# Performance work log

Hardware: AMD Instinct MI355X
Metric: run time of the kernel (lower is better)

The kernel has to match this reference:

```python
import jax, jax.numpy as jnp
import numpy as np
from jax import lax

C, NH, HC, HID, P = 192, 8, 64, 512, 16
B, H, W = 2, 128, 128
EPS = 1e-5


def setup_inputs() -> dict:
    key = jax.random.key(0)
    ks = jax.random.split(key, 12)
    f = lambda i, shape: jax.random.normal(ks[i], shape, jnp.float32) * 0.05
    return dict(
        x=jax.random.normal(ks[0], (B, C, H, W), jnp.float32),
        ln1_g=jnp.ones((C,), jnp.float32), ln1_b=jnp.zeros((C,), jnp.float32),
        wq=f(1, (HID, C)), wk=f(2, (HID, C)), wv=f(3, (HID, C)),
        wo=f(4, (C, HID)), bo=jnp.zeros((C,), jnp.float32),
        dw_w=f(5, (C, 1, 3, 3)), dw_b=jnp.zeros((C,), jnp.float32),
        mlp_w=f(6, (C, 2 * C)), mlp_b=jnp.zeros((C,), jnp.float32),
        ln2_g=jnp.ones((C,), jnp.float32), ln2_b=jnp.zeros((C,), jnp.float32),
        c1_w=f(7, (C, C)), c1_b=jnp.zeros((C,), jnp.float32),
        res_w=f(8, (C, 1, 3, 3)), res_b=jnp.zeros((C,), jnp.float32),
        c2_w=f(9, (C, C)), c2_b=jnp.zeros((C,), jnp.float32),
    )


def ln_ch(x, g, b):
    # LayerNorm over the channel dim of an NCHW tensor (biased variance, like torch)
    m = x.mean(1, keepdims=True)
    v = ((x - m) ** 2).mean(1, keepdims=True)
    return (x - m) / jnp.sqrt(v + EPS) * g[None, :, None, None] + b[None, :, None, None]


def inorm(x):
    # InstanceNorm2d, affine=False
    m = x.mean((2, 3), keepdims=True)
    v = ((x - m) ** 2).mean((2, 3), keepdims=True)
    return (x - m) / jnp.sqrt(v + EPS)


def conv1x1(x, w, b=None):
    y = jnp.einsum('oc,bchw->bohw', w, x)
    return y if b is None else y + b[None, :, None, None]


def dwconv(x, w, b):
    y = lax.conv_general_dilated(x, w, (1, 1), 'SAME',
                                 feature_group_count=x.shape[1],
                                 dimension_numbers=('NCHW', 'OIHW', 'NCHW'))
    return y + b[None, :, None, None]


def res_block(x, w, b):
    return jax.nn.gelu(inorm(dwconv(x, w, b)), approximate=False) + x


def dpsa(x, ln_g, ln_b, wq, wk, wv, wo, bo):
    Bs, _, Hs, Ws = x.shape
    xn = ln_ch(x, ln_g, ln_b)

    def proj(w):  # -> (B*NH, H, W, HC)
        t = jnp.einsum('oc,bchw->bohw', w, xn)
        return t.reshape(Bs * NH, HC, Hs, Ws).transpose(0, 2, 3, 1)

    l2n = lambda t: t / jnp.maximum(jnp.linalg.norm(t, axis=-1, keepdims=True), 1e-12)
    q = l2n(proj(wq))
    k = l2n(proj(wk))
    v = proj(wv)

    qs = q.sum((1, 2))                                   # (BH, HC)
    h_scores = jnp.einsum('bc,bhc->bh', qs, k.sum(2))    # (BH, H)
    w_scores = jnp.einsum('bc,bwc->bw', qs, k.sum(1))    # (BH, W)
    _, h_idx = lax.top_k(h_scores, P)
    _, w_idx = lax.top_k(w_scores, P)

    k = jnp.take_along_axis(k, h_idx[:, :, None, None], axis=1)   # (BH, P, W, HC)
    v = jnp.take_along_axis(v, h_idx[:, :, None, None], axis=1)
    k = jnp.take_along_axis(k, w_idx[:, None, :, None], axis=2)   # (BH, P, P, HC)
    v = jnp.take_along_axis(v, w_idx[:, None, :, None], axis=2)

    qf = q.reshape(Bs * NH, Hs * Ws, HC)
    kf = k.reshape(Bs * NH, P * P, HC)
    vf = v.reshape(Bs * NH, P * P, HC)
    attn = jax.nn.softmax(jnp.einsum('bqc,bkc->bqk', qf, kf), axis=-1)
    out = jnp.einsum('bqk,bkc->bqc', attn, vf)
    out = out.reshape(Bs, NH, Hs, Ws, HC).transpose(0, 1, 4, 2, 3).reshape(Bs, NH * HC, Hs, Ws)
    return conv1x1(out, wo, bo)


def reference(x, ln1_g, ln1_b, wq, wk, wv, wo, bo, dw_w, dw_b, mlp_w, mlp_b,
              ln2_g, ln2_b, c1_w, c1_b, res_w, res_b, c2_w, c2_b):
    global_branch = dpsa(x, ln1_g, ln1_b, wq, wk, wv, wo, bo)
    local_branch = dwconv(x, dw_w, dw_b)
    f = jnp.concatenate((local_branch, global_branch), axis=1)
    f = conv1x1(f, mlp_w, mlp_b) + x
    y = ln_ch(f, ln2_g, ln2_b)
    y = jax.nn.gelu(inorm(conv1x1(y, c1_w, c1_b)), approximate=False)
    y = res_block(y, res_w, res_b)
    y = inorm(conv1x1(y, c2_w, c2_b))
    return y
```

## Files before the change

kernel.cpp:

```cpp
#include <hip/hip_runtime.h>
#include <math.h>

constexpr int kC   = 192;
constexpr int kNH  = 8;
constexpr int kHC  = 64;
constexpr int kHID = 512;
constexpr int kP   = 16;
constexpr int kB   = 2;
constexpr int kH   = 128;
constexpr int kW   = 128;
constexpr int kHW  = kH * kW;
constexpr int kN   = kB * kHW;
constexpr float kEPS = 1e-5f;

typedef __attribute__((ext_vector_type(8))) short bf16x8;
typedef __attribute__((ext_vector_type(4))) float f32x4;

__device__ inline unsigned short f2bf(float f) {
    unsigned int u = __builtin_bit_cast(unsigned int, f);
    unsigned int r = (u + 0x7FFFu + ((u >> 16) & 1u)) >> 16;
    return (unsigned short)r;
}
__device__ inline float bf2f(unsigned short u) {
    return __builtin_bit_cast(float, (unsigned int)u << 16);
}
__device__ inline unsigned int cvtpk(float lo, float hi) {
    unsigned int r;
    asm("v_cvt_pk_bf16_f32 %0, %1, %2" : "=v"(r) : "v"(lo), "v"(hi));
    return r;
}
__device__ inline unsigned long long pk4(float a, float b, float c, float d) {
    return (unsigned long long)cvtpk(a, b) | ((unsigned long long)cvtpk(c, d) << 32);
}
__device__ inline f32x4 ubf4(unsigned long long u) {
    f32x4 r;
    r[0] = bf2f((unsigned short)u);
    r[1] = bf2f((unsigned short)(u >> 16));
    r[2] = bf2f((unsigned short)(u >> 32));
    r[3] = bf2f((unsigned short)(u >> 48));
    return r;
}

__global__ void prep_kernel(float* __restrict__ acc,
                            const float* wq, const float* wk, const float* wm,
                            const float* c1, const float* c2,
                            unsigned short* wqb, unsigned short* wkb,
                            unsigned short* mlpb1, unsigned short* c1b, unsigned short* c2b)
{
    int i = blockIdx.x * 256 + threadIdx.x;
    if (i < 2304) { acc[i] = 0.f; return; }
    i -= 2304;
    if (i < 98304) { wqb[i] = f2bf(wq[i]); return; }
    i -= 98304;
    if (i < 98304) { wkb[i] = f2bf(wk[i]); return; }
    i -= 98304;
    if (i < 36864) { int o = i / 192, k = i - o * 192; mlpb1[i] = f2bf(wm[o * 384 + k]); return; }
    i -= 36864;
    if (i < 36864) { c1b[i] = f2bf(c1[i]); return; }
    i -= 36864;
    if (i < 36864) { c2b[i] = f2bf(c2[i]); return; }
}

__global__ void wfuse_kernel(const float* __restrict__ mlp_w, const float* __restrict__ wo,
                             const float* __restrict__ mlp_b, const float* __restrict__ bo,
                             unsigned short* __restrict__ w2pb, float* __restrict__ bp2)
{
    int i = blockIdx.x * 256 + threadIdx.x;
    int o = i >> 9, j = i & 511;
    const float* a = mlp_w + o * 384 + 192;
    float s = 0.f;
    for (int c = 0; c < 192; ++c) s += a[c] * wo[c * 512 + j];
    w2pb[o * 512 + j] = f2bf(s);
    if (j == 0) {
        float t = mlp_b[o];
        for (int c = 0; c < 192; ++c) t += a[c] * bo[c];
        bp2[o] = t;
    }
}

__global__ __launch_bounds__(256) void txln_kernel(const float* __restrict__ x,
                                                   unsigned short* __restrict__ xpb,
                                                   unsigned short* __restrict__ xnb,
                                                   const float* __restrict__ g,
                                                   const float* __restrict__ bb)
{
    __shared__ float tile[192][65];
    __shared__ float red[2][4][64];
    __shared__ float pms[64], prs[64];
    int hw0 = blockIdx.x * 64;
    int b   = blockIdx.y;
    int tid = threadIdx.x;
    for (int i = tid; i < 192 * 64; i += 256) {
        int c = i >> 6, p = i & 63;
        tile[c][p] = x[(size_t)(b * kC + c) * kHW + hw0 + p];
    }
    __syncthreads();
    {
        int p = tid & 63, qt = tid >> 6;
        float s = 0.f, ss = 0.f;
// ... 54 lines not shown
#define MGEMM_CORE(KVAL, APTR, BPTR)                                              \
    {                                                                             \
        const unsigned short* Ap = APTR;                                          \
        const unsigned short* Bp = BPTR;                                          \
        _Pragma("unroll 2")                                                       \
        for (int k = 0; k < KVAL; k += 32) {                                      \
            bf16x8 a0 = *(const bf16x8*)(Ap + k);                                 \
            bf16x8 a1 = *(const bf16x8*)(Ap + (size_t)16 * KVAL + k);             \
            bf16x8 b0 = *(const bf16x8*)(Bp + k);                                 \
            bf16x8 b1 = *(const bf16x8*)(Bp + (size_t)16 * KVAL + k);             \
            bf16x8 b2 = *(const bf16x8*)(Bp + (size_t)32 * KVAL + k);             \
            bf16x8 b3 = *(const bf16x8*)(Bp + (size_t)48 * KVAL + k);             \
            acc[0][0] = __builtin_amdgcn_mfma_f32_16x16x32_bf16(a0, b0, acc[0][0], 0, 0, 0); \
            acc[0][1] = __builtin_amdgcn_mfma_f32_16x16x32_bf16(a0, b1, acc[0][1], 0, 0, 0); \
            acc[0][2] = __builtin_amdgcn_mfma_f32_16x16x32_bf16(a0, b2, acc[0][2], 0, 0, 0); \
            acc[0][3] = __builtin_amdgcn_mfma_f32_16x16x32_bf16(a0, b3, acc[0][3], 0, 0, 0); \
            acc[1][0] = __builtin_amdgcn_mfma_f32_16x16x32_bf16(a1, b0, acc[1][0], 0, 0, 0); \
            acc[1][1] = __builtin_amdgcn_mfma_f32_16x16x32_bf16(a1, b1, acc[1][1], 0, 0, 0); \
            acc[1][2] = __builtin_amdgcn_mfma_f32_16x16x32_bf16(a1, b2, acc[1][2], 0, 0, 0); \
            acc[1][3] = __builtin_amdgcn_mfma_f32_16x16x32_bf16(a1, b3, acc[1][3], 0, 0, 0); \
        }                                                                         \
    }

__global__ __launch_bounds__(256) void mgemm_is_kernel(
    const unsigned short* __restrict__ A, const unsigned short* __restrict__ B,
    unsigned short* __restrict__ out, const float* __restrict__ bias,
    float* __restrict__ accp)
{
    __shared__ float sa[2][64], qa[2][64];
    int nB = blockIdx.x * 128, oB = blockIdx.y * 64;
    int w = threadIdx.x >> 6, lane = threadIdx.x & 63;
    int l15 = lane & 15, g = lane >> 4;
    int wm = w & 1, wn = w >> 1;

    f32x4 acc[2][4];
#pragma unroll
    for (int mt = 0; mt < 2; ++mt)
#pragma unroll
        for (int nt = 0; nt < 4; ++nt) acc[mt][nt] = (f32x4){0.f,0.f,0.f,0.f};

    MGEMM_CORE(192, A + (size_t)(oB + wm * 32 + l15) * 192 + 8 * g,
                    B + (size_t)(nB + wn * 64 + l15) * 192 + 8 * g);

    f32x4 vv[2][4];
#pragma unroll
    for (int mt = 0; mt < 2; ++mt)
// ... 55 lines not shown

    f32x4 acc[2][4];
#pragma unroll
    for (int mt = 0; mt < 2; ++mt)
#pragma unroll
        for (int nt = 0; nt < 4; ++nt) acc[mt][nt] = (f32x4){0.f,0.f,0.f,0.f};

    MGEMM_CORE(192, A1 + (size_t)(oB + wm * 32 + l15) * 192 + 8 * g,
                    B1 + (size_t)(nB + wn * 64 + l15) * 192 + 8 * g);
    MGEMM_CORE(512, A2 + (size_t)(oB + wm * 32 + l15) * 512 + 8 * g,
                    B2 + (size_t)(nB + wn * 64 + l15) * 512 + 8 * g);

#pragma unroll
    for (int mt = 0; mt < 2; ++mt)
#pragma unroll
        for (int nt = 0; nt < 4; ++nt) {
            int o = oB + wm * 32 + mt * 16 + 4 * g;
            int n = nB + wn * 64 + nt * 16 + l15;
            f32x4 v = acc[mt][nt];
            v[0] += bp2[o]; v[1] += bp2[o+1]; v[2] += bp2[o+2]; v[3] += bp2[o+3];
            v += ubf4(*(const unsigned long long*)(res + (size_t)n * kC + o));
            *(unsigned long long*)(out + (size_t)n * kC + o) = pk4(v[0], v[1], v[2], v[3]);
        }
}

__global__ __launch_bounds__(256) void mgemm_l2_kernel(
    const unsigned short* __restrict__ A, const unsigned short* __restrict__ B,
    unsigned short* __restrict__ out, float* __restrict__ red_out)
{
    __shared__ float ssq[2][2][4][16];
    __shared__ float rbuf[2][2][4][2][4];
    int nB = blockIdx.x * 128, oB = blockIdx.y * 64;
    int w = threadIdx.x >> 6, lane = threadIdx.x & 63;
    int l15 = lane & 15, g = lane >> 4;
    int wm = w & 1, wn = w >> 1;

    f32x4 acc[2][4];
#pragma unroll
    for (int mt = 0; mt < 2; ++mt)
#pragma unroll
        for (int nt = 0; nt < 4; ++nt) acc[mt][nt] = (f32x4){0.f,0.f,0.f,0.f};

    MGEMM_CORE(192, A + (size_t)(oB + wm * 32 + l15) * 192 + 8 * g,
                    B + (size_t)(nB + wn * 64 + l15) * 192 + 8 * g);

#pragma unroll
    for (int nt = 0; nt < 4; ++nt) {
        float s = 0.f;
#pragma unroll
        for (int mt = 0; mt < 2; ++mt) {
            f32x4 a = acc[mt][nt];
            s += (a[0]*a[0] + a[1]*a[1]) + (a[2]*a[2] + a[3]*a[3]);
        }
        s += __shfl_xor(s, 16);
        s += __shfl_xor(s, 32);
        if (g == 0) ssq[wm][wn][nt][l15] = s;
    }
    __syncthreads();

    float sc[4];
#pragma unroll
    for (int nt = 0; nt < 4; ++nt) {
        float ss2 = ssq[0][wn][nt][l15] + ssq[1][wn][nt][l15];
        sc[nt] = 1.0f / fmaxf(sqrtf(ss2), 1e-12f);
    }

#pragma unroll
    for (int nt = 0; nt < 4; ++nt) {
        int n = nB + wn * 64 + nt * 16 + l15;
#pragma unroll
        for (int mt = 0; mt < 2; ++mt) {
            int o = oB + wm * 32 + mt * 16 + 4 * g;
            f32x4 v = acc[mt][nt];
            *(unsigned long long*)(out + (size_t)n * kHID + o) =
                pk4(v[0]*sc[nt], v[1]*sc[nt], v[2]*sc[nt], v[3]*sc[nt]);
        }
    }

    float sred[2][4] = {};
#pragma unroll
    for (int nt = 0; nt < 4; ++nt)
#pragma unroll
        for (int mt = 0; mt < 2; ++mt) {
            f32x4 a = acc[mt][nt];
            sred[mt][0] += a[0] * sc[nt];
            sred[mt][1] += a[1] * sc[nt];
            sred[mt][2] += a[2] * sc[nt];
            sred[mt][3] += a[3] * sc[nt];
        }
#pragma unroll
    for (int off = 1; off < 16; off <<= 1)
#pragma unroll
        for (int mt = 0; mt < 2; ++mt)
#pragma unroll
            for (int r = 0; r < 4; ++r)
                sred[mt][r] += __shfl_xor(sred[mt][r], off);
    if (l15 == 0)
#pragma unroll
        for (int mt = 0; mt < 2; ++mt)
#pragma unroll
            for (int r = 0; r < 4; ++r)
                rbuf[wm][wn][g][mt][r] = sred[mt][r];
    __syncthreads();
    if (threadIdx.x < 64) {
        int o = threadIdx.x;
        int wm2 = o >> 5, mt2 = (o >> 4) & 1, g2 = (o >> 2) & 3, r2 = o & 3;
        float v = rbuf[wm2][0][g2][mt2][r2] + rbuf[wm2][1][g2][mt2][r2];
        int row = (nB & (kHW - 1)) >> 7;
        int b = nB >> 14;
        int bh = b * 8 + blockIdx.y;
        red_out[((size_t)(bh * 128 + row)) * 64 + o] = v;
    }
}

__global__ void sum_h_kernel(const unsigned short* __restrict__ buf, float* __restrict__ out)
{
    __shared__ float red[4][64];
    int w = blockIdx.x, bh = blockIdx.y;
    int hc = threadIdx.x & 63, seg = threadIdx.x >> 6;
    int b = bh >> 3, nh = bh & 7;
    const unsigned short* p = buf + (size_t)(b * kHW + seg * 32 * kW + w) * kHID + nh * kHC + hc;
    float s = 0.f;
    for (int h = 0; h < 32; ++h) s += bf2f(p[(size_t)h * kW * kHID]);
    red[seg][hc] = s;
    __syncthreads();
    if (threadIdx.x < 64)
        out[((size_t)bh * kW + w) * kHC + threadIdx.x] =
            red[0][threadIdx.x] + red[1][threadIdx.x] + red[2][threadIdx.x] + red[3][threadIdx.x];
}

__global__ void score_topk_kernel(const float* __restrict__ qpart,
                                  const float* __restrict__ ksum_h,
                                  const float* __restrict__ ksum_w,
                                  int* __restrict__ hidx, int* __restrict__ widx)
{
    __shared__ float qsl[2][64];
    __shared__ float hs[128], ws[128];
    int bh = blockIdx.x;
    int tid = threadIdx.x;
    int hc = tid & 63, grp = tid >> 6;
    {
        const float* qp = qpart + ((size_t)bh * 128 + grp * 64) * 64 + hc;
        float s = 0.f;
        for (int i = 0; i < 64; ++i) s += qp[(size_t)i * 64];
        qsl[grp][hc] = s;
    }
    __syncthreads();
    if (tid < 64) qsl[0][tid] += qsl[1][tid];
    __syncthreads();
    {
        const float* kh = ksum_h + ((size_t)bh * 128 + tid) * 64;
// ... 8 lines not shown
    }
    __syncthreads();
    int sel = tid >> 6;
    const float* sc = sel ? ws : hs;
    int* out = (sel ? widx : hidx) + bh * kP;
    int lane = tid & 63;
    float v0 = sc[lane], v1 = sc[lane + 64];
    int i0 = lane, i1 = lane + 64;
    for (int p = 0; p < kP; ++p) {
        float bv; int bi;
        if (v1 > v0) { bv = v1; bi = i1; } else { bv = v0; bi = i0; }
#pragma unroll
        for (int off = 1; off < 64; off <<= 1) {
            float ov = __shfl_xor(bv, off);
            int   oi = __shfl_xor(bi, off);
            if (ov > bv || (ov == bv && oi < bi)) { bv = ov; bi = oi; }
        }
        if (lane == 0) out[p] = bi;
        if (i0 == bi) v0 = -INFINITY;
        if (i1 == bi) v1 = -INFINITY;
    }
}

__global__ void gather_kv_kernel(const unsigned short* __restrict__ kpb,
                                 const unsigned short* __restrict__ xnb,
                                 const float* __restrict__ wv,
                                 const int* __restrict__ hidx, const int* __restrict__ widx,
                                 unsigned short* __restrict__ kf, unsigned short* __restrict__ vfT)
{
    int bh = blockIdx.y, p1 = blockIdx.x;
    int b = bh >> 3, nh = bh & 7;
    int hc = threadIdx.x & 63, pg = threadIdx.x >> 6;
    int hrow = hidx[bh * kP + p1];
    int o = nh * kHC + hc;
    const float* wvp = wv + (size_t)o * kC;
    for (int p2 = pg; p2 < kP; p2 += 4) {
        int wcol = widx[bh * kP + p2];
        int n = b * kHW + hrow * kW + wcol;
        int kidx = p1 * kP + p2;
        kf[((size_t)bh * 256 + kidx) * 64 + hc] = kpb[(size_t)n * kHID + nh * kHC + hc];
        const unsigned int* xr = (const unsigned int*)(xnb + (size_t)n * kC);
        float s = 0.f;
        for (int c2 = 0; c2 < kC / 2; ++c2) {
            unsigned int u = xr[c2];
            s += wvp[c2 * 2]     * bf2f((unsigned short)(u & 0xffff));
            s += wvp[c2 * 2 + 1] * bf2f((unsigned short)(u >> 16));
        }
        vfT[((size_t)bh * 64 + hc) * 256 + kidx] = f2bf(s);
    }
}

__global__ __launch_bounds__(256) void attn_kernel(
    const unsigned short* __restrict__ qpb, unsigned short* __restrict__ ob,
    const unsigned short* __restrict__ kf, const unsigned short* __restrict__ vfT)
{
    __shared__ unsigned short pls[64 * 256];
    __shared__ float lred[4][4][16];

    int bh = blockIdx.y; int b = bh >> 3, nh = bh & 7;
    int n0 = b * kHW + blockIdx.x * 64;
    int tid = threadIdx.x;
    int w = tid >> 6, lane = tid & 63, l15 = lane & 15, g = lane >> 4;

    bf16x8 bq[4][2];
#pragma unroll
    for (int nt = 0; nt < 4; ++nt)
#pragma unroll
        for (int kt = 0; kt < 2; ++kt)
            bq[nt][kt] = *(const bf16x8*)(qpb + (size_t)(n0 + nt * 16 + l15) * kHID
                                          + nh * kHC + kt * 32 + 8 * g);

    const unsigned short* kfb = kf + (size_t)bh * 256 * 64;
    bf16x8 ak[4][2];
#pragma unroll
    for (int mt = 0; mt < 4; ++mt)
#pragma unroll
        for (int kt = 0; kt < 2; ++kt)
            ak[mt][kt] = *(const bf16x8*)&kfb[(size_t)(w * 64 + mt * 16 + l15) * 64 + kt * 32 + 8 * g];

    f32x4 acc[4][4];
#pragma unroll
    for (int mt = 0; mt < 4; ++mt)
#pragma unroll
        for (int nt = 0; nt < 4; ++nt) acc[mt][nt] = (f32x4){0.f,0.f,0.f,0.f};

#pragma unroll
    for (int kt = 0; kt < 2; ++kt)
#pragma unroll
        for (int mt = 0; mt < 4; ++mt)
#pragma unroll
            for (int nt = 0; nt < 4; ++nt)
                acc[mt][nt] = __builtin_amdgcn_mfma_f32_16x16x32_bf16(
                    ak[mt][kt], bq[nt][kt], acc[mt][nt], 0, 0, 0);

    float lpart[4] = {0.f, 0.f, 0.f, 0.f};
#pragma unroll
    for (int mt = 0; mt < 4; ++mt)
#pragma unroll
        for (int nt = 0; nt < 4; ++nt) {
            float e0 = __expf(acc[mt][nt][0]);
            float e1 = __expf(acc[mt][nt][1]);
            float e2 = __expf(acc[mt][nt][2]);
            float e3 = __expf(acc[mt][nt][3]);
            lpart[nt] += (e0 + e1) + (e2 + e3);
            int qq = nt * 16 + l15;
            int k0 = w * 64 + mt * 16 + 4 * g;
            int kx = k0 ^ ((qq & 7) << 3);
            *(unsigned long long*)&pls[qq * 256 + kx] = pk4(e0, e1, e2, e3);
        }
#pragma unroll
    for (int nt = 0; nt < 4; ++nt) {
        lpart[nt] += __shfl_xor(lpart[nt], 16);
        lpart[nt] += __shfl_xor(lpart[nt], 32);
    }
    if (g == 0)
#pragma unroll
        for (int nt = 0; nt < 4; ++nt) lred[w][nt][l15] = lpart[nt];
    __syncthreads();

    const unsigned short* vfb = vfT + (size_t)bh * 64 * 256;
    f32x4 oacc[4];
#pragma unroll
    for (int nt = 0; nt < 4; ++nt) oacc[nt] = (f32x4){0.f,0.f,0.f,0.f};

#pragma unroll
    for (int ks = 0; ks < 8; ++ks) {
        bf16x8 av = *(const bf16x8*)&vfb[(size_t)(w * 16 + l15) * 256 + ks * 32 + 8 * g];
#pragma unroll
        for (int nt = 0; nt < 4; ++nt) {
            int qq = nt * 16 + l15;
            int kx = (ks * 32 + 8 * g) ^ ((qq & 7) << 3);
            bf16x8 bp = *(const bf16x8*)&pls[qq * 256 + kx];
            oacc[nt] = __builtin_amdgcn_mfma_f32_16x16x32_bf16(av, bp, oacc[nt], 0, 0, 0);
        }
    }

#pragma unroll
    for (int nt = 0; nt < 4; ++nt) {
        float l = lred[0][nt][l15] + lred[1][nt][l15] + lred[2][nt][l15] + lred[3][nt][l15];
        float inv = 1.0f / l;
        int qq = nt * 16 + l15;
        int hc0 = w * 16 + 4 * g;
        *(unsigned long long*)(ob + (size_t)(n0 + qq) * kHID + nh * kHC + hc0) =
            pk4(oacc[nt][0] * inv, oacc[nt][1] * inv, oacc[nt][2] * inv, oacc[nt][3] * inv);
    }
}

__global__ void dwconv_pm_kernel(const unsigned short* __restrict__ in,
                                 unsigned short* __restrict__ out,
                                 const float* __restrict__ wt, const float* __restrict__ bias)
{
    int idx = blockIdx.x * 256 + threadIdx.x;
    int n = idx / 48;
    int c0 = (idx - n * 48) * 4;
    int hw = n & (kHW - 1);
    int h = hw >> 7, ww = hw & 127;
    f32x4 s = *(const f32x4*)(bias + c0);
#pragma unroll
    for (int dy = -1; dy <= 1; ++dy) {
        int hh = h + dy;
        if (hh < 0 || hh >= kH) continue;
#pragma unroll
        for (int dx = -1; dx <= 1; ++dx) {
            int wx = ww + dx;
            if (wx < 0 || wx >= kW) continue;
            f32x4 v = ubf4(*(const unsigned long long*)(in + (size_t)(n + dy * kW + dx) * kC + c0));
            int t = (dy + 1) * 3 + (dx + 1);
            s[0] += v[0] * wt[(c0 + 0) * 9 + t];
            s[1] += v[1] * wt[(c0 + 1) * 9 + t];
            s[2] += v[2] * wt[(c0 + 2) * 9 + t];
            s[3] += v[3] * wt[(c0 + 3) * 9 + t];
        }
    }
    *(unsigned long long*)(out + (size_t)n * kC + c0) = pk4(s[0], s[1], s[2], s[3]);
}

__global__ void istats_bf16_kernel(const unsigned short* __restrict__ in, float* __restrict__ acc)
{
    int n0 = blockIdx.x * 64;
    int b = n0 >> 14;
    int c = threadIdx.x;
    float s = 0.f, ss = 0.f;
    for (int p = 0; p < 64; ++p) {
        float v = bf2f(in[(size_t)(n0 + p) * kC + c]);
        s += v; ss += v * v;
    }
    atomicAdd(&acc[(size_t)(b * kC + c) * 2],     s);
    atomicAdd(&acc[(size_t)(b * kC + c) * 2 + 1], ss);
}

__device__ inline void inorm_ms(const float* acc, int b, int c, float& m, float& rs)
{
    float s  = acc[(size_t)(b * kC + c) * 2];
    float ss = acc[(size_t)(b * kC + c) * 2 + 1];
    m = s * (1.0f / kHW);
    float var = ss * (1.0f / kHW) - m * m;
    rs = rsqrtf(var + kEPS);
}

template<int MODE>
__global__ void apply_pm_kernel(const unsigned short* __restrict__ in, const float* __restrict__ acc,
                                unsigned short* __restrict__ out, const unsigned short* __restrict__ addsrc)
{
    int idx = blockIdx.x * 256 + threadIdx.x;
    int n = idx / 48;
    int c0 = (idx - n * 48) * 4;
    int b = n >> 14;
    f32x4 v = ubf4(*(const unsigned long long*)(in + (size_t)n * kC + c0));
    f32x4 r;
#pragma unroll
    for (int j = 0; j < 4; ++j) {
        float m, rs;
        inorm_ms(acc, b, c0 + j, m, rs);
        float x = (v[j] - m) * rs;
        r[j] = 0.5f * x * (1.0f + erff(x * 0.70710678118654752f));
    }
    if (MODE == 1)
        r += ubf4(*(const unsigned long long*)(addsrc + (size_t)n * kC + c0));
    *(unsigned long long*)(out + (size_t)n * kC + c0) = pk4(r[0], r[1], r[2], r[3]);
}

__global__ __launch_bounds__(256) void final_kernel(const unsigned short* __restrict__ in,
                                                    const float* __restrict__ acc,
                                                    float* __restrict__ out)
{
    __shared__ unsigned short tile[192][68];
    int n0 = blockIdx.x * 64;
    int b = n0 >> 14;
    int hw0 = n0 & (kHW - 1);
    int tid = threadIdx.x;
    for (int i = tid; i < 64 * 48; i += 256) {
        int p = i / 48, cq = i - p * 48;
        unsigned long long u = *(const unsigned long long*)(in + (size_t)(n0 + p) * kC + cq * 4);
        tile[cq * 4 + 0][p] = (unsigned short)u;
        tile[cq * 4 + 1][p] = (unsigned short)(u >> 16);
        tile[cq * 4 + 2][p] = (unsigned short)(u >> 32);
        tile[cq * 4 + 3][p] = (unsigned short)(u >> 48);
    }
    __syncthreads();
    for (int i = tid; i < 192 * 16; i += 256) {
        int c = i >> 4, grp = i & 15;
        float m, rs;
// ... 17 lines not shown
    const float* wk    = (const float*)d_in[4];
    const float* wv    = (const float*)d_in[5];
    const float* wo    = (const float*)d_in[6];
    const float* bo    = (const float*)d_in[7];
    const float* dw_w  = (const float*)d_in[8];
    const float* dw_b  = (const float*)d_in[9];
    const float* mlp_w = (const float*)d_in[10];
    const float* mlp_b = (const float*)d_in[11];
    const float* ln2_g = (const float*)d_in[12];
    const float* ln2_b = (const float*)d_in[13];
    const float* c1_w  = (const float*)d_in[14];
    const float* c1_b  = (const float*)d_in[15];
    const float* res_w = (const float*)d_in[16];
    const float* res_b = (const float*)d_in[17];
    const float* c2_w  = (const float*)d_in[18];
    const float* c2_b  = (const float*)d_in[19];

    char* base = (char*)d_ws;
    unsigned short* XPb = (unsigned short*)(base);
    unsigned short* XNb = (unsigned short*)(base + 25165824);
    unsigned short* QPb = (unsigned short*)(base + 37748736);
    unsigned short* F   = QPb;
    unsigned short* T2  = QPb;
    unsigned short* KPb = (unsigned short*)(base + 71303168);
    unsigned short* OB  = KPb;
    unsigned short* Y2  = KPb;
    unsigned short* LB  = (unsigned short*)(base + 104857600);
    unsigned short* Y3  = LB;
    unsigned short* T1  = (unsigned short*)(base + 117440512);
    unsigned short* R   = T1;
    char* sm = base + 130023424;
    float* qpart  = (float*)(sm);                 sm += 524288;
    float* ksum_h = (float*)(sm);                 sm += 524288;
    float* ksum_w = (float*)(sm);                 sm += 524288;
    float* acc0   = (float*)(sm);                 sm += 3072;
    float* acc1   = (float*)(sm);                 sm += 3072;
    float* acc2   = (float*)(sm);                 sm += 3072;
    unsigned short* kf   = (unsigned short*)(sm); sm += 524288;
    unsigned short* vfT  = (unsigned short*)(sm); sm += 524288;
    unsigned short* wqb  = (unsigned short*)(sm); sm += 196608;
    unsigned short* wkb  = (unsigned short*)(sm); sm += 196608;
    unsigned short* mlpb1= (unsigned short*)(sm); sm += 73728;
    unsigned short* c1b  = (unsigned short*)(sm); sm += 73728;
    unsigned short* c2b  = (unsigned short*)(sm); sm += 73728;
    unsigned short* w2pb = (unsigned short*)(sm); sm += 196608;
    float* bp2 = (float*)(sm);                    sm += 1024;
    int* hidx = (int*)(sm);                       sm += 1024;
    int* widx = (int*)(sm);

    prep_kernel<<<1209, 256, 0, stream>>>(acc0, wq, wk, mlp_w, c1_w, c2_w,
                                          wqb, wkb, mlpb1, c1b, c2b);
    wfuse_kernel<<<384, 256, 0, stream>>>(mlp_w, wo, mlp_b, bo, w2pb, bp2);
    txln_kernel<<<dim3(kHW / 64, kB), 256, 0, stream>>>(x, XPb, XNb, ln1_g, ln1_b);

    mgemm_l2_kernel<<<dim3(kN / 128, kNH), 256, 0, stream>>>(wqb, XNb, QPb, qpart);
    mgemm_l2_kernel<<<dim3(kN / 128, kNH), 256, 0, stream>>>(wkb, XNb, KPb, ksum_h);
    sum_h_kernel<<<dim3(kW, 16), 256, 0, stream>>>(KPb, ksum_w);
    score_topk_kernel<<<16, 128, 0, stream>>>(qpart, ksum_h, ksum_w, hidx, widx);
    gather_kv_kernel<<<dim3(kP, 16), 256, 0, stream>>>(KPb, XNb, wv, hidx, widx, kf, vfT);
    attn_kernel<<<dim3(kHW / 64, 16), 256, 0, stream>>>(QPb, OB, kf, vfT);

    dwconv_pm_kernel<<<(kN * 48) / 256, 256, 0, stream>>>(XPb, LB, dw_w, dw_b);
    mgemm_mlp_kernel<<<dim3(kN / 128, kC / 64), 256, 0, stream>>>(mlpb1, LB, w2pb, OB, F, bp2, XPb);

    ln_pm_bf16_kernel<<<(kN * 4) / 256, 256, 0, stream>>>(F, XNb, ln2_g, ln2_b);
    mgemm_is_kernel<<<dim3(kN / 128, kC / 64), 256, 0, stream>>>(c1b, XNb, T1, c1_b, acc0);
    apply_pm_kernel<0><<<(kN * 48) / 256, 256, 0, stream>>>(T1, acc0, Y2, nullptr);
    dwconv_pm_kernel<<<(kN * 48) / 256, 256, 0, stream>>>(Y2, R, res_w, res_b);
    istats_bf16_kernel<<<kN / 64, 192, 0, stream>>>(R, acc1);
    apply_pm_kernel<1><<<(kN * 48) / 256, 256, 0, stream>>>(R, acc1, Y3, Y2);
    mgemm_is_kernel<<<dim3(kN / 128, kC / 64), 256, 0, stream>>>(c2b, Y3, T2, c2_b, acc2);
    final_kernel<<<kN / 64, 256, 0, stream>>>(T2, acc2, (float*)d_out);
}
```

Before: 490.0 us.

## Fuse branch GEMMs and dwconv, drop K-projection buffer, fold GELU into convs

```diff
diff --git a/kernel.cpp b/kernel.cpp
--- a/kernel.cpp
+++ b/kernel.cpp
@@ -40,16 +40,21 @@
     r[3] = bf2f((unsigned short)(u >> 48));
     return r;
 }
-
-__global__ void prep_kernel(float* __restrict__ acc,
+__device__ inline float gelu_f(float x) {
+    return 0.5f * x * (1.0f + erff(x * 0.70710678118654752f));
+}
+
+__global__ void prep_kernel(float* __restrict__ zbase,
                             const float* wq, const float* wk, const float* wm,
                             const float* c1, const float* c2,
+                            const float* wo, const float* mlp_b, const float* bo,
                             unsigned short* wqb, unsigned short* wkb,
-                            unsigned short* mlpb1, unsigned short* c1b, unsigned short* c2b)
+                            unsigned short* mlpb1, unsigned short* c1b, unsigned short* c2b,
+                            unsigned short* w2pb, float* bp2)
 {
     int i = blockIdx.x * 256 + threadIdx.x;
-    if (i < 2304) { acc[i] = 0.f; return; }
-    i -= 2304;
+    if (i < 133376) { zbase[i] = 0.f; return; }
+    i -= 133376;
     if (i < 98304) { wqb[i] = f2bf(wq[i]); return; }
     i -= 98304;
     if (i < 98304) { wkb[i] = f2bf(wk[i]); return; }
@@ -59,22 +64,18 @@
     if (i < 36864) { c1b[i] = f2bf(c1[i]); return; }
     i -= 36864;
     if (i < 36864) { c2b[i] = f2bf(c2[i]); return; }
-}
-
-__global__ void wfuse_kernel(const float* __restrict__ mlp_w, const float* __restrict__ wo,
-                             const float* __restrict__ mlp_b, const float* __restrict__ bo,
-                             unsigned short* __restrict__ w2pb, float* __restrict__ bp2)
-{
-    int i = blockIdx.x * 256 + threadIdx.x;
-    int o = i >> 9, j = i & 511;
-    const float* a = mlp_w + o * 384 + 192;
-    float s = 0.f;
-    for (int c = 0; c < 192; ++c) s += a[c] * wo[c * 512 + j];
-    w2pb[o * 512 + j] = f2bf(s);
-    if (j == 0) {
-        float t = mlp_b[o];
-        for (int c = 0; c < 192; ++c) t += a[c] * bo[c];
-        bp2[o] = t;
+    i -= 36864;
+    if (i < 98304) {
+        int o = i >> 9, j = i & 511;
+        const float* a = wm + o * 384 + 192;
+        float s = 0.f;
+        for (int c = 0; c < 192; ++c) s += a[c] * wo[c * 512 + j];
+        w2pb[o * 512 + j] = f2bf(s);
+        if (j == 0) {
+            float t = mlp_b[o];
+            for (int c = 0; c < 192; ++c) t += a[c] * bo[c];
+            bp2[o] = t;
+        }
     }
 }
 
@@ -175,6 +176,155 @@
         }                                                                         \
     }
 
+template<int IS_K>
+__device__ void mgemm_l2_body(int nblk, int head,
+                              const unsigned short* __restrict__ A,
+                              const unsigned short* __restrict__ B,
+                              unsigned short* __restrict__ out,
+                              float* __restrict__ red_out,
+                              float* __restrict__ ksum_w)
+{
+    __shared__ float ssq[2][2][4][16];
+    __shared__ float rbuf[2][2][4][2][4];
+    int nB = nblk * 128, oB = head * 64;
+    int w = threadIdx.x >> 6, lane = threadIdx.x & 63;
+    int l15 = lane & 15, g = lane >> 4;
+    int wm = w & 1, wn = w >> 1;
+
+    f32x4 acc[2][4];
+#pragma unroll
+    for (int mt = 0; mt < 2; ++mt)
+#pragma unroll
+        for (int nt = 0; nt < 4; ++nt) acc[mt][nt] = (f32x4){0.f,0.f,0.f,0.f};
+
+    MGEMM_CORE(192, A + (size_t)(oB + wm * 32 + l15) * 192 + 8 * g,
+                    B + (size_t)(nB + wn * 64 + l15) * 192 + 8 * g);
+
+#pragma unroll
+    for (int nt = 0; nt < 4; ++nt) {
+        float s = 0.f;
+#pragma unroll
+        for (int mt = 0; mt < 2; ++mt) {
+            f32x4 a = acc[mt][nt];
+            s += (a[0]*a[0] + a[1]*a[1]) + (a[2]*a[2] + a[3]*a[3]);
+        }
+        s += __shfl_xor(s, 16);
+        s += __shfl_xor(s, 32);
+        if (g == 0) ssq[wm][wn][nt][l15] = s;
+    }
+    __syncthreads();
+
+    float sc[4];
+#pragma unroll
+    for (int nt = 0; nt < 4; ++nt) {
+        float ss2 = ssq[0][wn][nt][l15] + ssq[1][wn][nt][l15];
+        sc[nt] = 1.0f / fmaxf(sqrtf(ss2), 1e-12f);
+    }
+
+    int b = nB >> 14;
+    int bh = b * 8 + head;
+#pragma unroll
+    for (int nt = 0; nt < 4; ++nt) {
+        int n = nB + wn * 64 + nt * 16 + l15;
+#pragma unroll
+        for (int mt = 0; mt < 2; ++mt) {
+            int o = oB + wm * 32 + mt * 16 + 4 * g;
+            f32x4 v = acc[mt][nt];
+            if (IS_K) {
+                int ww = n & (kW - 1);
+                float* dst = ksum_w + ((size_t)(bh * kW + ww)) * 64 + (o & 63);
+                atomicAdd(dst + 0, v[0] * sc[nt]);
+                atomicAdd(dst + 1, v[1] * sc[nt]);
+                atomicAdd(dst + 2, v[2] * sc[nt]);
+                atomicAdd(dst + 3, v[3] * sc[nt]);
+            } else {
+                *(unsigned long long*)(out + (size_t)n * kHID + o) =
+                    pk4(v[0]*sc[nt], v[1]*sc[nt], v[2]*sc[nt], v[3]*sc[nt]);
+            }
+        }
+    }
+
+    float sred[2][4] = {};
+#pragma unroll
+    for (int nt = 0; nt < 4; ++nt)
+#pragma unroll
+        for (int mt = 0; mt < 2; ++mt) {
+            f32x4 a = acc[mt][nt];
+            sred[mt][0] += a[0] * sc[nt];
+            sred[mt][1] += a[1] * sc[nt];
+            sred[mt][2] += a[2] * sc[nt];
+            sred[mt][3] += a[3] * sc[nt];
+        }
+#pragma unroll
+    for (int off = 1; off < 16; off <<= 1)
+#pragma unroll
+        for (int mt = 0; mt < 2; ++mt)
+#pragma unroll
+            for (int r = 0; r < 4; ++r)
+                sred[mt][r] += __shfl_xor(sred[mt][r], off);
+    if (l15 == 0)
+#pragma unroll
+        for (int mt = 0; mt < 2; ++mt)
+#pragma unroll
+            for (int r = 0; r < 4; ++r)
+                rbuf[wm][wn][g][mt][r] = sred[mt][r];
+    __syncthreads();
+    if (threadIdx.x < 64) {
+        int o = threadIdx.x;
+        int wm2 = o >> 5, mt2 = (o >> 4) & 1, g2 = (o >> 2) & 3, r2 = o & 3;
+        float v = rbuf[wm2][0][g2][mt2][r2] + rbuf[wm2][1][g2][mt2][r2];
+        int row = (nB & (kHW - 1)) >> 7;
+        red_out[((size_t)(bh * 128 + row)) * 64 + o] = v;
+    }
+}
+
+__device__ void dwconv_body(int idx, const unsigned short* __restrict__ in,
+                            unsigned short* __restrict__ out,
+                            const float* __restrict__ wt, const float* __restrict__ bias)
+{
+    int n = idx / 48;
+    int c0 = (idx - n * 48) * 4;
+    int hw = n & (kHW - 1);
+    int h = hw >> 7, ww = hw & 127;
+    f32x4 s = *(const f32x4*)(bias + c0);
+#pragma unroll
+    for (int dy = -1; dy <= 1; ++dy) {
+        int hh = h + dy;
+        if (hh < 0 || hh >= kH) continue;
+#pragma unroll
+        for (int dx = -1; dx <= 1; ++dx) {
+            int wx = ww + dx;
+            if (wx < 0 || wx >= kW) continue;
+            f32x4 v = ubf4(*(const unsigned long long*)(in + (size_t)(n + dy * kW + dx) * kC + c0));
+            int t = (dy + 1) * 3 + (dx + 1);
+            s[0] += v[0] * wt[(c0 + 0) * 9 + t];
+            s[1] += v[1] * wt[(c0 + 1) * 9 + t];
+            s[2] += v[2] * wt[(c0 + 2) * 9 + t];
+            s[3] += v[3] * wt[(c0 + 3) * 9 + t];
+        }
+    }
+    *(unsigned long long*)(out + (size_t)n * kC + c0) = pk4(s[0], s[1], s[2], s[3]);
+}
+
+__global__ __launch_bounds__(256) void branch_kernel(
+    const unsigned short* __restrict__ wqb, const unsigned short* __restrict__ wkb,
+    const unsigned short* __restrict__ xnb, const unsigned short* __restrict__ xpb,
+    unsigned short* __restrict__ qpb, float* __restrict__ qpart,
+    float* __restrict__ ksum_h, float* __restrict__ ksum_w,
+    unsigned short* __restrict__ lb,
+    const float* __restrict__ dw_w, const float* __restrict__ dw_b)
+{
+    int id = blockIdx.x;
+    if (id < 2048) {
+        mgemm_l2_body<0>(id & 255, id >> 8, wqb, xnb, qpb, qpart, nullptr);
+    } else if (id < 4096) {
+        id -= 2048;
+        mgemm_l2_body<1>(id & 255, id >> 8, wkb, xnb, nullptr, ksum_h, ksum_w);
+    } else {
+        dwconv_body((id - 4096) * 256 + threadIdx.x, xpb, lb, dw_w, dw_b);
+    }
+}
+
 __global__ __launch_bounds__(256) void mgemm_is_kernel(
     const unsigned short* __restrict__ A, const unsigned short* __restrict__ B,
     unsigned short* __restrict__ out, const float* __restrict__ bias,
@@ -276,111 +426,6 @@
             v += ubf4(*(const unsigned long long*)(res + (size_t)n * kC + o));
             *(unsigned long long*)(out + (size_t)n * kC + o) = pk4(v[0], v[1], v[2], v[3]);
         }
-}
-
-__global__ __launch_bounds__(256) void mgemm_l2_kernel(
-    const unsigned short* __restrict__ A, const unsigned short* __restrict__ B,
-    unsigned short* __restrict__ out, float* __restrict__ red_out)
-{
-    __shared__ float ssq[2][2][4][16];
-    __shared__ float rbuf[2][2][4][2][4];
-    int nB = blockIdx.x * 128, oB = blockIdx.y * 64;
-    int w = threadIdx.x >> 6, lane = threadIdx.x & 63;
-    int l15 = lane & 15, g = lane >> 4;
-    int wm = w & 1, wn = w >> 1;
-
-    f32x4 acc[2][4];
-#pragma unroll
-    for (int mt = 0; mt < 2; ++mt)
-#pragma unroll
-        for (int nt = 0; nt < 4; ++nt) acc[mt][nt] = (f32x4){0.f,0.f,0.f,0.f};
-
-    MGEMM_CORE(192, A + (size_t)(oB + wm * 32 + l15) * 192 + 8 * g,
-                    B + (size_t)(nB + wn * 64 + l15) * 192 + 8 * g);
-
-#pragma unroll
-    for (int nt = 0; nt < 4; ++nt) {
-        float s = 0.f;
-#pragma unroll
-        for (int mt = 0; mt < 2; ++mt) {
-            f32x4 a = acc[mt][nt];
-            s += (a[0]*a[0] + a[1]*a[1]) + (a[2]*a[2] + a[3]*a[3]);
-        }
-        s += __shfl_xor(s, 16);
-        s += __shfl_xor(s, 32);
-        if (g == 0) ssq[wm][wn][nt][l15] = s;
-    }
-    __syncthreads();
-
-    float sc[4];
-#pragma unroll
-    for (int nt = 0; nt < 4; ++nt) {
-        float ss2 = ssq[0][wn][nt][l15] + ssq[1][wn][nt][l15];
-        sc[nt] = 1.0f / fmaxf(sqrtf(ss2), 1e-12f);
-    }
-
-#pragma unroll
-    for (int nt = 0; nt < 4; ++nt) {
-        int n = nB + wn * 64 + nt * 16 + l15;
-#pragma unroll
-        for (int mt = 0; mt < 2; ++mt) {
-            int o = oB + wm * 32 + mt * 16 + 4 * g;
-            f32x4 v = acc[mt][nt];
-            *(unsigned long long*)(out + (size_t)n * kHID + o) =
-                pk4(v[0]*sc[nt], v[1]*sc[nt], v[2]*sc[nt], v[3]*sc[nt]);
-        }
-    }
-
-    float sred[2][4] = {};
-#pragma unroll
-    for (int nt = 0; nt < 4; ++nt)
-#pragma unroll
-        for (int mt = 0; mt < 2; ++mt) {
-            f32x4 a = acc[mt][nt];
-            sred[mt][0] += a[0] * sc[nt];
-            sred[mt][1] += a[1] * sc[nt];
-            sred[mt][2] += a[2] * sc[nt];
-            sred[mt][3] += a[3] * sc[nt];
-        }
-#pragma unroll
-    for (int off = 1; off < 16; off <<= 1)
-#pragma unroll
-        for (int mt = 0; mt < 2; ++mt)
-#pragma unroll
-            for (int r = 0; r < 4; ++r)
-                sred[mt][r] += __shfl_xor(sred[mt][r], off);
-    if (l15 == 0)
-#pragma unroll
-        for (int mt = 0; mt < 2; ++mt)
-#pragma unroll
-            for (int r = 0; r < 4; ++r)
-                rbuf[wm][wn][g][mt][r] = sred[mt][r];
-    __syncthreads();
-    if (threadIdx.x < 64) {
-        int o = threadIdx.x;
-        int wm2 = o >> 5, mt2 = (o >> 4) & 1, g2 = (o >> 2) & 3, r2 = o & 3;
-        float v = rbuf[wm2][0][g2][mt2][r2] + rbuf[wm2][1][g2][mt2][r2];
-        int row = (nB & (kHW - 1)) >> 7;
-        int b = nB >> 14;
-        int bh = b * 8 + blockIdx.y;
-        red_out[((size_t)(bh * 128 + row)) * 64 + o] = v;
-    }
-}
-
-__global__ void sum_h_kernel(const unsigned short* __restrict__ buf, float* __restrict__ out)
-{
-    __shared__ float red[4][64];
-    int w = blockIdx.x, bh = blockIdx.y;
-    int hc = threadIdx.x & 63, seg = threadIdx.x >> 6;
-    int b = bh >> 3, nh = bh & 7;
-    const unsigned short* p = buf + (size_t)(b * kHW + seg * 32 * kW + w) * kHID + nh * kHC + hc;
-    float s = 0.f;
-    for (int h = 0; h < 32; ++h) s += bf2f(p[(size_t)h * kW * kHID]);
-    red[seg][hc] = s;
-    __syncthreads();
-    if (threadIdx.x < 64)
-        out[((size_t)bh * kW + w) * kHC + threadIdx.x] =
-            red[0][threadIdx.x] + red[1][threadIdx.x] + red[2][threadIdx.x] + red[3][threadIdx.x];
 }
 
 __global__ void score_topk_kernel(const float* __restrict__ qpart,
@@ -435,7 +480,7 @@
     }
 }
 
-__global__ void gather_kv_kernel(const unsigned short* __restrict__ kpb,
+__global__ void gather_kv_kernel(const unsigned short* __restrict__ wkb,
                                  const unsigned short* __restrict__ xnb,
                                  const float* __restrict__ wv,
                                  const int* __restrict__ hidx, const int* __restrict__ widx,
@@ -447,19 +492,29 @@
     int hrow = hidx[bh * kP + p1];
     int o = nh * kHC + hc;
     const float* wvp = wv + (size_t)o * kC;
+    const unsigned short* wkp = wkb + (size_t)o * kC;
     for (int p2 = pg; p2 < kP; p2 += 4) {
         int wcol = widx[bh * kP + p2];
         int n = b * kHW + hrow * kW + wcol;
         int kidx = p1 * kP + p2;
-        kf[((size_t)bh * 256 + kidx) * 64 + hc] = kpb[(size_t)n * kHID + nh * kHC + hc];
         const unsigned int* xr = (const unsigned int*)(xnb + (size_t)n * kC);
-        float s = 0.f;
+        const unsigned int* kr = (const unsigned int*)wkp;
+        float sv = 0.f, sk = 0.f;
         for (int c2 = 0; c2 < kC / 2; ++c2) {
             unsigned int u = xr[c2];
-            s += wvp[c2 * 2]     * bf2f((unsigned short)(u & 0xffff));
-            s += wvp[c2 * 2 + 1] * bf2f((unsigned short)(u >> 16));
-        }
-        vfT[((size_t)bh * 64 + hc) * 256 + kidx] = f2bf(s);
+            float x0 = bf2f((unsigned short)(u & 0xffff));
+            float x1 = bf2f((unsigned short)(u >> 16));
+            sv += wvp[c2 * 2] * x0 + wvp[c2 * 2 + 1] * x1;
+            unsigned int kw2 = kr[c2];
+            sk += bf2f((unsigned short)(kw2 & 0xffff)) * x0
+                + bf2f((unsigned short)(kw2 >> 16)) * x1;
+        }
+        float ss = sk * sk;
+#pragma unroll
+        for (int off = 1; off < 64; off <<= 1) ss += __shfl_xor(ss, off);
+        float sc = 1.0f / fmaxf(sqrtf(ss), 1e-12f);
+        kf[((size_t)bh * 256 + kidx) * 64 + hc] = f2bf(sk * sc);
+        vfT[((size_t)bh * 64 + hc) * 256 + kidx] = f2bf(sv);
     }
 }
 
@@ -471,18 +526,10 @@
     __shared__ float lred[4][4][16];
 
     int bh = blockIdx.y; int b = bh >> 3, nh = bh & 7;
-    int n0 = b * kHW + blockIdx.x * 64;
+    int nbase = b * kHW + blockIdx.x * 128;
     int tid = threadIdx.x;
     int w = tid >> 6, lane = tid & 63, l15 = lane & 15, g = lane >> 4;
 
-    bf16x8 bq[4][2];
-#pragma unroll
-    for (int nt = 0; nt < 4; ++nt)
-#pragma unroll
-        for (int kt = 0; kt < 2; ++kt)
-            bq[nt][kt] = *(const bf16x8*)(qpb + (size_t)(n0 + nt * 16 + l15) * kHID
-                                          + nh * kHC + kt * 32 + 8 * g);
-
     const unsigned short* kfb = kf + (size_t)bh * 256 * 64;
     bf16x8 ak[4][2];
 #pragma unroll
@@ -491,101 +538,87 @@
         for (int kt = 0; kt < 2; ++kt)
             ak[mt][kt] = *(const bf16x8*)&kfb[(size_t)(w * 64 + mt * 16 + l15) * 64 + kt * 32 + 8 * g];
 
-    f32x4 acc[4][4];
-#pragma unroll
-    for (int mt = 0; mt < 4; ++mt)
-#pragma unroll
-        for (int nt = 0; nt < 4; ++nt) acc[mt][nt] = (f32x4){0.f,0.f,0.f,0.f};
-
-#pragma unroll
-    for (int kt = 0; kt < 2; ++kt)
+    const unsigned short* vfb = vfT + (size_t)bh * 64 * 256;
+
+#pragma unroll
+    for (int sub = 0; sub < 2; ++sub) {
+        int n0 = nbase + sub * 64;
+        bf16x8 bq[4][2];
+#pragma unroll
+        for (int nt = 0; nt < 4; ++nt)
+#pragma unroll
+            for (int kt = 0; kt < 2; ++kt)
+                bq[nt][kt] = *(const bf16x8*)(qpb + (size_t)(n0 + nt * 16 + l15) * kHID
+                                              + nh * kHC + kt * 32 + 8 * g);
+
+        f32x4 acc[4][4];
 #pragma unroll
         for (int mt = 0; mt < 4; ++mt)
 #pragma unroll
-            for (int nt = 0; nt < 4; ++nt)
-                acc[mt][nt] = __builtin_amdgcn_mfma_f32_16x16x32_bf16(
-                    ak[mt][kt], bq[nt][kt], acc[mt][nt], 0, 0, 0);
-
-    float lpart[4] = {0.f, 0.f, 0.f, 0.f};
-#pragma unroll
-    for (int mt = 0; mt < 4; ++mt)
+            for (int nt = 0; nt < 4; ++nt) acc[mt][nt] = (f32x4){0.f,0.f,0.f,0.f};
+
+#pragma unroll
+        for (int kt = 0; kt < 2; ++kt)
+#pragma unroll
+            for (int mt = 0; mt < 4; ++mt)
+#pragma unroll
+                for (int nt = 0; nt < 4; ++nt)
+                    acc[mt][nt] = __builtin_amdgcn_mfma_f32_16x16x32_bf16(
+                        ak[mt][kt], bq[nt][kt], acc[mt][nt], 0, 0, 0);
+
+        if (sub) __syncthreads();
+
+        float lpart[4] = {0.f, 0.f, 0.f, 0.f};
+#pragma unroll
+        for (int mt = 0; mt < 4; ++mt)
+#pragma unroll
+            for (int nt = 0; nt < 4; ++nt) {
+                float e0 = __expf(acc[mt][nt][0]);
+                float e1 = __expf(acc[mt][nt][1]);
+                float e2 = __expf(acc[mt][nt][2]);
+                float e3 = __expf(acc[mt][nt][3]);
+                lpart[nt] += (e0 + e1) + (e2 + e3);
+                int qq = nt * 16 + l15;
+                int k0 = w * 64 + mt * 16 + 4 * g;
+                int kx = k0 ^ ((qq & 7) << 3);
+                *(unsigned long long*)&pls[qq * 256 + kx] = pk4(e0, e1, e2, e3);
+            }
 #pragma unroll
         for (int nt = 0; nt < 4; ++nt) {
-            float e0 = __expf(acc[mt][nt][0]);
-            float e1 = __expf(acc[mt][nt][1]);
-            float e2 = __expf(acc[mt][nt][2]);
-            float e3 = __expf(acc[mt][nt][3]);
-            lpart[nt] += (e0 + e1) + (e2 + e3);
+            lpart[nt] += __shfl_xor(lpart[nt], 16);
+            lpart[nt] += __shfl_xor(lpart[nt], 32);
+        }
+        if (g == 0)
+#pragma unroll
+            for (int nt = 0; nt < 4; ++nt) lred[w][nt][l15] = lpart[nt];
+        __syncthreads();
+
+        f32x4 oacc[4];
+#pragma unroll
+        for (int nt = 0; nt < 4; ++nt) oacc[nt] = (f32x4){0.f,0.f,0.f,0.f};
+
+#pragma unroll
+        for (int ks = 0; ks < 8; ++ks) {
+            bf16x8 av = *(const bf16x8*)&vfb[(size_t)(w * 16 + l15) * 256 + ks * 32 + 8 * g];
+#pragma unroll
+            for (int nt = 0; nt < 4; ++nt) {
+                int qq = nt * 16 + l15;
+                int kx = (ks * 32 + 8 * g) ^ ((qq & 7) << 3);
+                bf16x8 bp = *(const bf16x8*)&pls[qq * 256 + kx];
+                oacc[nt] = __builtin_amdgcn_mfma_f32_16x16x32_bf16(av, bp, oacc[nt], 0, 0, 0);
+            }
+        }
+
+#pragma unroll
+        for (int nt = 0; nt < 4; ++nt) {
+            float l = lred[0][nt][l15] + lred[1][nt][l15] + lred[2][nt][l15] + lred[3][nt][l15];
+            float inv = 1.0f / l;
             int qq = nt * 16 + l15;
-            int k0 = w * 64 + mt * 16 + 4 * g;
-            int kx = k0 ^ ((qq & 7) << 3);
-            *(unsigned long long*)&pls[qq * 256 + kx] = pk4(e0, e1, e2, e3);
-        }
-#pragma unroll
-    for (int nt = 0; nt < 4; ++nt) {
-        lpart[nt] += __shfl_xor(lpart[nt], 16);
-        lpart[nt] += __shfl_xor(lpart[nt], 32);
-    }
-    if (g == 0)
-#pragma unroll
-        for (int nt = 0; nt < 4; ++nt) lred[w][nt][l15] = lpart[nt];
-    __syncthreads();
-
-    const unsigned short* vfb = vfT + (size_t)bh * 64 * 256;
-    f32x4 oacc[4];
-#pragma unroll
-    for (int nt = 0; nt < 4; ++nt) oacc[nt] = (f32x4){0.f,0.f,0.f,0.f};
-
-#pragma unroll
-    for (int ks = 0; ks < 8; ++ks) {
-        bf16x8 av = *(const bf16x8*)&vfb[(size_t)(w * 16 + l15) * 256 + ks * 32 + 8 * g];
-#pragma unroll
-        for (int nt = 0; nt < 4; ++nt) {
-            int qq = nt * 16 + l15;
-            int kx = (ks * 32 + 8 * g) ^ ((qq & 7) << 3);
-            bf16x8 bp = *(const bf16x8*)&pls[qq * 256 + kx];
-            oacc[nt] = __builtin_amdgcn_mfma_f32_16x16x32_bf16(av, bp, oacc[nt], 0, 0, 0);
-        }
-    }
-
-#pragma unroll
-    for (int nt = 0; nt < 4; ++nt) {
-        float l = lred[0][nt][l15] + lred[1][nt][l15] + lred[2][nt][l15] + lred[3][nt][l15];
-        float inv = 1.0f / l;
-        int qq = nt * 16 + l15;
-        int hc0 = w * 16 + 4 * g;
-        *(unsigned long long*)(ob + (size_t)(n0 + qq) * kHID + nh * kHC + hc0) =
-            pk4(oacc[nt][0] * inv, oacc[nt][1] * inv, oacc[nt][2] * inv, oacc[nt][3] * inv);
-    }
-}
-
-__global__ void dwconv_pm_kernel(const unsigned short* __restrict__ in,
-                                 unsigned short* __restrict__ out,
-                                 const float* __restrict__ wt, const float* __restrict__ bias)
-{
-    int idx = blockIdx.x * 256 + threadIdx.x;
-    int n = idx / 48;
-    int c0 = (idx - n * 48) * 4;
-    int hw = n & (kHW - 1);
-    int h = hw >> 7, ww = hw & 127;
-    f32x4 s = *(const f32x4*)(bias + c0);
-#pragma unroll
-    for (int dy = -1; dy <= 1; ++dy) {
-        int hh = h + dy;
-        if (hh < 0 || hh >= kH) continue;
-#pragma unroll
-        for (int dx = -1; dx <= 1; ++dx) {
-            int wx = ww + dx;
-            if (wx < 0 || wx >= kW) continue;
-            f32x4 v = ubf4(*(const unsigned long long*)(in + (size_t)(n + dy * kW + dx) * kC + c0));
-            int t = (dy + 1) * 3 + (dx + 1);
-            s[0] += v[0] * wt[(c0 + 0) * 9 + t];
-            s[1] += v[1] * wt[(c0 + 1) * 9 + t];
-            s[2] += v[2] * wt[(c0 + 2) * 9 + t];
-            s[3] += v[3] * wt[(c0 + 3) * 9 + t];
-        }
-    }
-    *(unsigned long long*)(out + (size_t)n * kC + c0) = pk4(s[0], s[1], s[2], s[3]);
+            int hc0 = w * 16 + 4 * g;
+            *(unsigned long long*)(ob + (size_t)(n0 + qq) * kHID + nh * kHC + hc0) =
+                pk4(oacc[nt][0] * inv, oacc[nt][1] * inv, oacc[nt][2] * inv, oacc[nt][3] * inv);
+        }
+    }
 }
 
 __global__ void istats_bf16_kernel(const unsigned short* __restrict__ in, float* __restrict__ acc)
@@ -611,26 +644,59 @@
     rs = rsqrtf(var + kEPS);
 }
 
-template<int MODE>
-__global__ void apply_pm_kernel(const unsigned short* __restrict__ in, const float* __restrict__ acc,
-                                unsigned short* __restrict__ out, const unsigned short* __restrict__ addsrc)
+__global__ void dwconv_gelu_kernel(const unsigned short* __restrict__ t1,
+                                   const float* __restrict__ acc0,
+                                   unsigned short* __restrict__ rout,
+                                   const float* __restrict__ wt, const float* __restrict__ bias)
+{
+    int idx = blockIdx.x * 256 + threadIdx.x;
+    int n = idx / 48;
+    int c0 = (idx - n * 48) * 4;
+    int hw = n & (kHW - 1);
+    int b = n >> 14;
+    int h = hw >> 7, ww = hw & 127;
+    float m[4], rs[4];
+#pragma unroll
+    for (int j = 0; j < 4; ++j) inorm_ms(acc0, b, c0 + j, m[j], rs[j]);
+    f32x4 s = *(const f32x4*)(bias + c0);
+#pragma unroll
+    for (int dy = -1; dy <= 1; ++dy) {
+        int hh = h + dy;
+        if (hh < 0 || hh >= kH) continue;
+#pragma unroll
+        for (int dx = -1; dx <= 1; ++dx) {
+            int wx = ww + dx;
+            if (wx < 0 || wx >= kW) continue;
+            f32x4 v = ubf4(*(const unsigned long long*)(t1 + (size_t)(n + dy * kW + dx) * kC + c0));
+            int t = (dy + 1) * 3 + (dx + 1);
+#pragma unroll
+            for (int j = 0; j < 4; ++j)
+                s[j] += gelu_f((v[j] - m[j]) * rs[j]) * wt[(c0 + j) * 9 + t];
+        }
+    }
+    *(unsigned long long*)(rout + (size_t)n * kC + c0) = pk4(s[0], s[1], s[2], s[3]);
+}
+
+__global__ void apply_res_kernel(const unsigned short* __restrict__ r,
+                                 const unsigned short* __restrict__ t1,
+                                 const float* __restrict__ acc1, const float* __restrict__ acc0,
+                                 unsigned short* __restrict__ out)
 {
     int idx = blockIdx.x * 256 + threadIdx.x;
     int n = idx / 48;
     int c0 = (idx - n * 48) * 4;
     int b = n >> 14;
-    f32x4 v = ubf4(*(const unsigned long long*)(in + (size_t)n * kC + c0));
-    f32x4 r;
+    f32x4 vr = ubf4(*(const unsigned long long*)(r  + (size_t)n * kC + c0));
+    f32x4 vt = ubf4(*(const unsigned long long*)(t1 + (size_t)n * kC + c0));
+    f32x4 o;
 #pragma unroll
     for (int j = 0; j < 4; ++j) {
-        float m, rs;
-        inorm_ms(acc, b, c0 + j, m, rs);
-        float x = (v[j] - m) * rs;
-        r[j] = 0.5f * x * (1.0f + erff(x * 0.70710678118654752f));
-    }
-    if (MODE == 1)
-        r += ubf4(*(const unsigned long long*)(addsrc + (size_t)n * kC + c0));
-    *(unsigned long long*)(out + (size_t)n * kC + c0) = pk4(r[0], r[1], r[2], r[3]);
+        float m1, rs1, m0, rs0;
+        inorm_ms(acc1, b, c0 + j, m1, rs1);
+        inorm_ms(acc0, b, c0 + j, m0, rs0);
+        o[j] = gelu_f((vr[j] - m1) * rs1) + gelu_f((vt[j] - m0) * rs0);
+    }
+    *(unsigned long long*)(out + (size_t)n * kC + c0) = pk4(o[0], o[1], o[2], o[3]);
 }
 
 __global__ __launch_bounds__(256) void final_kernel(const unsigned short* __restrict__ in,
@@ -694,20 +760,18 @@
     unsigned short* QPb = (unsigned short*)(base + 37748736);
     unsigned short* F   = QPb;
     unsigned short* T2  = QPb;
-    unsigned short* KPb = (unsigned short*)(base + 71303168);
-    unsigned short* OB  = KPb;
-    unsigned short* Y2  = KPb;
+    unsigned short* OB  = (unsigned short*)(base + 71303168);
+    unsigned short* R   = OB;
     unsigned short* LB  = (unsigned short*)(base + 104857600);
     unsigned short* Y3  = LB;
     unsigned short* T1  = (unsigned short*)(base + 117440512);
-    unsigned short* R   = T1;
     char* sm = base + 130023424;
     float* qpart  = (float*)(sm);                 sm += 524288;
     float* ksum_h = (float*)(sm);                 sm += 524288;
-    float* ksum_w = (float*)(sm);                 sm += 524288;
     float* acc0   = (float*)(sm);                 sm += 3072;
     float* acc1   = (float*)(sm);                 sm += 3072;
     float* acc2   = (float*)(sm);                 sm += 3072;
+    float* ksum_w = (float*)(sm);                 sm += 524288;
     unsigned short* kf   = (unsigned short*)(sm); sm += 524288;
     unsigned short* vfT  = (unsigned short*)(sm); sm += 524288;
     unsigned short* wqb  = (unsigned short*)(sm); sm += 196608;
@@ -720,27 +784,21 @@
     int* hidx = (int*)(sm);                       sm += 1024;
     int* widx = (int*)(sm);
 
-    prep_kernel<<<1209, 256, 0, stream>>>(acc0, wq, wk, mlp_w, c1_w, c2_w,
-                                          wqb, wkb, mlpb1, c1b, c2b);
-    wfuse_kernel<<<384, 256, 0, stream>>>(mlp_w, wo, mlp_b, bo, w2pb, bp2);
+    prep_kernel<<<2111, 256, 0, stream>>>(acc0, wq, wk, mlp_w, c1_w, c2_w,
+                                          wo, mlp_b, bo,
+                                          wqb, wkb, mlpb1, c1b, c2b, w2pb, bp2);
     txln_kernel<<<dim3(kHW / 64, kB), 256, 0, stream>>>(x, XPb, XNb, ln1_g, ln1_b);
-
-    mgemm_l2_kernel<<<dim3(kN / 128, kNH), 256, 0, stream>>>(wqb, XNb, QPb, qpart);
-    mgemm_l2_kernel<<<dim3(kN / 128, kNH), 256, 0, stream>>>(wkb, XNb, KPb, ksum_h);
-    sum_h_kernel<<<dim3(kW, 16), 256, 0, stream>>>(KPb, ksum_w);
+    branch_kernel<<<10240, 256, 0, stream>>>(wqb, wkb, XNb, XPb, QPb, qpart,
+                                             ksum_h, ksum_w, LB, dw_w, dw_b);
     score_topk_kernel<<<16, 128, 0, stream>>>(qpart, ksum_h, ksum_w, hidx, widx);
-    gather_kv_kernel<<<dim3(kP, 16), 256, 0, stream>>>(KPb, XNb, wv, hidx, widx, kf, vfT);
-    attn_kernel<<<dim3(kHW / 64, 16), 256, 0, stream>>>(QPb, OB, kf, vfT);
-
-    dwconv_pm_kernel<<<(kN * 48) / 256, 256, 0, stream>>>(XPb, LB, dw_w, dw_b);
+    gather_kv_kernel<<<dim3(kP, 16), 256, 0, stream>>>(wkb, XNb, wv, hidx, widx, kf, vfT);
+    attn_kernel<<<dim3(kHW / 128, 16), 256, 0, stream>>>(QPb, OB, kf, vfT);
     mgemm_mlp_kernel<<<dim3(kN / 128, kC / 64), 256, 0, stream>>>(mlpb1, LB, w2pb, OB, F, bp2, XPb);
-
     ln_pm_bf16_kernel<<<(kN * 4) / 256, 256, 0, stream>>>(F, XNb, ln2_g, ln2_b);
     mgemm_is_kernel<<<dim3(kN / 128, kC / 64), 256, 0, stream>>>(c1b, XNb, T1, c1_b, acc0);
-    apply_pm_kernel<0><<<(kN * 48) / 256, 256, 0, stream>>>(T1, acc0, Y2, nullptr);
-    dwconv_pm_kernel<<<(kN * 48) / 256, 256, 0, stream>>>(Y2, R, res_w, res_b);
+    dwconv_gelu_kernel<<<(kN * 48) / 256, 256, 0, stream>>>(T1, acc0, R, res_w, res_b);
     istats_bf16_kernel<<<kN / 64, 192, 0, stream>>>(R, acc1);
-    apply_pm_kernel<1><<<(kN * 48) / 256, 256, 0, stream>>>(R, acc1, Y3, Y2);
+    apply_res_kernel<<<(kN * 48) / 256, 256, 0, stream>>>(R, T1, acc1, acc0, Y3);
     mgemm_is_kernel<<<dim3(kN / 128, kC / 64), 256, 0, stream>>>(c2b, Y3, T2, c2_b, acc2);
     final_kernel<<<kN / 64, 256, 0, stream>>>(T2, acc2, (float*)d_out);
 }
```

Measured after the change: 696.3 us. +42.1%, slower.
